# Kernel tuning notes

Hardware: AMD Instinct MI355X
Metric: run time of the kernel (lower is better)

Reference implementation:

```python
import jax, jax.numpy as jnp
import numpy as np

NUM_ENT = 14541; NUM_REL = 237; NUM_EDGES = 544230
D = 200; B = 2048
IPERM = 1; IK_H = 20; IK_W = 10; NFILT = 96; KER = 9
FLAT = IK_H * 2 * IK_W * NFILT * IPERM
LEAKY = 0.2; EPS = 1e-5


def _chequer_perm(rng):
    # faithful reimplementation of RagatInteractE.get_chequer_perm
    ent_perm = np.stack([rng.permutation(D) for _ in range(IPERM)])
    rel_perm = np.stack([rng.permutation(D) for _ in range(IPERM)])
    comb = []
    for k in range(IPERM):
        temp = []; ei = 0; ri = 0
        for i in range(IK_H):
            for j in range(IK_W):
                ent_first = (k % 2 == 0) == (i % 2 == 0)
                if ent_first:
                    temp.append(ent_perm[k, ei]); ei += 1
                    temp.append(rel_perm[k, ri] + D); ri += 1
                else:
                    temp.append(rel_perm[k, ri] + D); ri += 1
                    temp.append(ent_perm[k, ei]); ei += 1
        comb.append(temp)
    return jnp.asarray(np.asarray(comb, dtype=np.int32))


def _bn1d(x, g, b):  # [N, C], training-mode batch stats (torch default)
    m = x.mean(0); v = x.var(0)
    return (x - m) / jnp.sqrt(v + EPS) * g + b


def _bn2d(x, g, b):  # [N, C, H, W]
    m = x.mean((0, 2, 3), keepdims=True); v = x.var((0, 2, 3), keepdims=True)
    return (x - m) / jnp.sqrt(v + EPS) * g[None, :, None, None] + b[None, :, None, None]


def _seg_softmax_agg(score, msg, seg, n):
    # segment softmax over edges grouped by destination node, then weighted scatter-add
    mx = jax.ops.segment_max(score, seg, num_segments=n)
    ex = jnp.exp(score - mx[seg])
    den = jax.ops.segment_sum(ex, seg, num_segments=n)
    alpha = ex / (den[seg] + 1e-16)
    return jax.ops.segment_sum(msg * alpha[:, None], seg, num_segments=n)


def setup_inputs() -> dict:
    key = jax.random.key(0)
    ks = jax.random.split(key, 20)
    f = lambda k, shp, s=0.1: jax.random.normal(k, shp, jnp.float32) * s
    rng = np.random.RandomState(0)
    return {
        'init_embed': f(ks[0], (NUM_ENT, D)),
        'init_rel': f(ks[1], (2 * NUM_REL, D)),
        'loop_rel': f(ks[2], (1, D)),
        'w_in': f(ks[3], (D, D)),
        'w_out': f(ks[4], (D, D)),
        'w_loop': f(ks[5], (D, D)),
        'w_rel': f(ks[6], (D, D)),
        'att_in': f(ks[7], (D,)),
        'att_out': f(ks[8], (D,)),
        'bn_conv_g': jnp.ones((D,), jnp.float32),
        'bn_conv_b': jnp.zeros((D,), jnp.float32),
        'conv_filt': f(ks[9], (NFILT, 1, KER, KER)),
        'bn0_g': jnp.ones((IPERM,), jnp.float32),
        'bn0_b': jnp.zeros((IPERM,), jnp.float32),
        'bn1_g': jnp.ones((NFILT * IPERM,), jnp.float32),
        'bn1_b': jnp.zeros((NFILT * IPERM,), jnp.float32),
        'fc_w': f(ks[10], (FLAT, D), 0.02),
        'fc_b': jnp.zeros((D,), jnp.float32),
        'bn2_g': jnp.ones((D,), jnp.float32),
        'bn2_b': jnp.zeros((D,), jnp.float32),
        'bias': jnp.zeros((NUM_ENT,), jnp.float32),
        'edge_index': jax.random.randint(ks[11], (2, NUM_EDGES), 0, NUM_ENT, jnp.int32),
        'edge_type': jnp.concatenate([
            jax.random.randint(ks[12], (NUM_EDGES // 2,), 0, NUM_REL, jnp.int32),
            jax.random.randint(ks[13], (NUM_EDGES // 2,), NUM_REL, 2 * NUM_REL, jnp.int32)]),
        'sub': jax.random.randint(ks[14], (B,), 0, NUM_ENT, jnp.int32),
        'rel': jax.random.randint(ks[15], (B,), 0, 2 * NUM_REL, jnp.int32),
        'chequer_perm': _chequer_perm(rng),
    }


def reference(init_embed, init_rel, loop_rel, w_in, w_out, w_loop, w_rel,
              att_in, att_out, bn_conv_g, bn_conv_b, conv_filt,
              bn0_g, bn0_b, bn1_g, bn1_b, fc_w, fc_b, bn2_g, bn2_b, bias,
              edge_index, edge_type, sub, rel, chequer_perm):
    # --- RagatConv (1 layer): relation-aware composition + edge attention + scatter-agg ---
    rel_full = jnp.concatenate([init_rel, loop_rel], 0)
    src, dst = edge_index[0], edge_index[1]
    comp = init_embed[dst] * rel_full[edge_type]          # [E, D] mult composition
    half = NUM_EDGES // 2
    msg_in = comp[:half] @ w_in                           # [E/2, D]
    msg_out = comp[half:] @ w_out
    s_in = jax.nn.leaky_relu((msg_in * att_in).sum(-1), LEAKY)
    s_out = jax.nn.leaky_relu((msg_out * att_out).sum(-1), LEAKY)
    agg_in = _seg_softmax_agg(s_in, msg_in, src[:half], NUM_ENT)
    agg_out = _seg_softmax_agg(s_out, msg_out, src[half:], NUM_ENT)
    loop_msg = (init_embed * loop_rel[0]) @ w_loop
    ent = (agg_in + agg_out + loop_msg) / 3.0
    ent = jnp.tanh(_bn1d(ent, bn_conv_g, bn_conv_b))      # [num_ent, D]
    rel_out = init_rel @ w_rel                            # [2*num_rel, D]

    # --- InteractE chequer-perm circular-conv scoring ---
    comb = jnp.concatenate([ent[sub], rel_out[rel]], 1)   # [B, 2D]
    cheq = comb[:, chequer_perm]                          # [B, IPERM, 2D]
    x = cheq.reshape(B, IPERM, 2 * IK_W, IK_H)
    x = _bn2d(x, bn0_g, bn0_b)
    p = KER // 2
    x = jnp.concatenate([x[..., -p:, :], x, x[..., :p, :]], axis=2)  # circular pad H
    x = jnp.concatenate([x[..., -p:], x, x[..., :p]], axis=3)        # circular pad W
    kern = jnp.tile(conv_filt, (IPERM, 1, 1, 1))          # [NFILT*IPERM, 1, K, K]
    x = jax.lax.conv_general_dilated(x, kern, (1, 1), 'VALID',
                                     dimension_numbers=('NCHW', 'OIHW', 'NCHW'),
                                     feature_group_count=IPERM)       # [B, 96, 20, 20]
    x = jax.nn.relu(_bn2d(x, bn1_g, bn1_b))
    x = x.reshape(B, FLAT)
    x = x @ fc_w + fc_b
    x = jax.nn.relu(_bn1d(x, bn2_g, bn2_b))               # [B, D]
    scores = x @ ent.T + bias                              # one_to_n scoring
    return jax.nn.sigmoid(scores)
```

## Files before the change

kernel.cpp:

```cpp
#include <hip/hip_runtime.h>
#include <hip/hip_bf16.h>

constexpr int DV     = 200;
constexpr int N_ENT  = 14541;
constexpr int N_EDGE = 544230;
constexpr int HALF_E = N_EDGE / 2;
constexpr int NSEG   = 2 * N_ENT;
constexpr int BB     = 2048;
constexpr int NF     = 96;
constexpr int FLATN  = 38400;
constexpr float LEAK = 0.2f;
constexpr float BEPS = 1e-5f;

typedef unsigned int u32;
typedef unsigned short u16;
typedef __attribute__((ext_vector_type(8))) short bf16x8;
typedef __attribute__((ext_vector_type(4))) float f32x4;
typedef __attribute__((ext_vector_type(4))) unsigned short u16x4;

constexpr size_t OFF_S    = 0;
constexpr size_t OFF_EID  = 544230;
constexpr size_t OFF_CNT  = 1088460;
constexpr size_t OFF_OFFS = 1117542;
constexpr size_t OFF_AGG  = 1146624;
constexpr size_t OFF_FC   = 6963218;
constexpr size_t ZERO_BEG = OFF_CNT;
constexpr size_t ZERO_END = OFF_FC + 409600;
constexpr size_t OFF_V    = 7372818;
constexpr size_t OFF_WTH  = 0;
constexpr size_t OFF_ENTH = 3840000;
constexpr size_t OFF_ENTL = 5352264;
constexpr size_t OFF_WTL  = 7373220;
constexpr size_t OFF_EMB  = 7373218;
constexpr size_t OFF_EPRE = 10281418;
constexpr size_t OFF_ENT  = 13189618;
constexpr size_t OFF_RELO = 16097818;
constexpr size_t OFF_CM   = 16192618;
constexpr size_t OFF_CV   = 16192818;
constexpr size_t OFF_CHEQ = 16193018;
constexpr size_t OFF_YH   = 16193020;
constexpr size_t OFF_YL   = 16406012;
constexpr size_t OFF_P0   = 17012218;
constexpr size_t OFF_ST0  = 17016314;
constexpr size_t OFF_CHP  = 17016316;
constexpr size_t OFF_B1SC = 17409532;
constexpr size_t OFF_B1BI = 17409628;
constexpr size_t OFF_XC   = 17819324;
constexpr size_t WS_WORDS = OFF_XC + 39321600;

__device__ inline float bf2f(u16 u) { return __uint_as_float(((u32)u) << 16); }
__device__ inline u16 f2bf(float f) {
    __hip_bfloat16 h = __float2bfloat16(f);
    return *reinterpret_cast<u16*>(&h);
}
__device__ inline void gl_lds16(const void* g, void* l) {
    __builtin_amdgcn_global_load_lds(
        (const __attribute__((address_space(1))) void*)g,
        (__attribute__((address_space(3))) void*)l, 16, 0, 0);
}

__global__ void k_vatt(const float* __restrict__ w_in, const float* __restrict__ w_out,
                       const float* __restrict__ att_in, const float* __restrict__ att_out,
                       float* __restrict__ v) {
    int t = blockIdx.x * 256 + threadIdx.x;
    if (t < DV) {
        float s = 0.f;
        for (int j = 0; j < DV; ++j) s += w_in[t * DV + j] * att_in[j];
        v[t] = s;
    } else if (t < 2 * DV) {
        int k = t - DV;
        float s = 0.f;
        for (int j = 0; j < DV; ++j) s += w_out[k * DV + j] * att_out[j];
        v[t] = s;
    }
}

__global__ void k_edge_score(const float* __restrict__ embed, const float* __restrict__ rel,
                             const int* __restrict__ eidx, const int* __restrict__ etype,
                             const float* __restrict__ v, float* __restrict__ s_all) {
    int gw = (blockIdx.x * 256 + threadIdx.x) >> 6;
    int lane = threadIdx.x & 63;
    if (gw >= N_EDGE) return;
    int e = gw;
    int dst = eidx[N_EDGE + e], et = etype[e];
    int dir = (e >= HALF_E);
    const float* vv = v + dir * DV;
    const float* er = embed + (size_t)dst * DV;
    const float* rr = rel + (size_t)et * DV;
    float acc = 0.f;
    for (int d = lane; d < DV; d += 64) acc += er[d] * rr[d] * vv[d];
    for (int off = 32; off > 0; off >>= 1) acc += __shfl_down(acc, off);
    if (lane == 0) {
        float s = acc > 0.f ? acc : LEAK * acc;
        s_all[e] = s;
    }
}

__global__ void k_hist(const int* __restrict__ eidx, u32* __restrict__ cnt) {
    int e = blockIdx.x * 256 + threadIdx.x;
    if (e >= N_EDGE) return;
    int seg = (e >= HALF_E ? N_ENT : 0) + eidx[e];
    atomicAdd(&cnt[seg], 1u);
}

__global__ void k_scan(u32* __restrict__ cnt, u32* __restrict__ offs) {
    __shared__ u32 s[256];
    __shared__ u32 base;
    if (threadIdx.x == 0) base = 0;
    __syncthreads();
    for (int c0 = 0; c0 < NSEG; c0 += 256) {
        int i = c0 + threadIdx.x;
        u32 vv = (i < NSEG) ? cnt[i] : 0;
        s[threadIdx.x] = vv;
        __syncthreads();
        for (int o = 1; o < 256; o <<= 1) {
            u32 t = (threadIdx.x >= (u32)o) ? s[threadIdx.x - o] : 0u;
            __syncthreads();
            s[threadIdx.x] += t;
            __syncthreads();
        }
        u32 exc = base + s[threadIdx.x] - vv;
        if (i < NSEG) { offs[i] = exc; cnt[i] = exc; }
        __syncthreads();
        if (threadIdx.x == 255) base += s[255];
        __syncthreads();
    }
}

__global__ void k_scatter(const int* __restrict__ eidx, u32* __restrict__ pos,
                          u32* __restrict__ eid) {
    int e = blockIdx.x * 256 + threadIdx.x;
    if (e >= N_EDGE) return;
    int seg = (e >= HALF_E ? N_ENT : 0) + eidx[e];
    u32 slot = atomicAdd(&pos[seg], 1u);
    eid[slot] = (u32)e;
}

__global__ void k_seg_agg(const float* __restrict__ embed, const float* __restrict__ rel,
                          const int* __restrict__ eidx, const int* __restrict__ etype,
                          const float* __restrict__ s_all, const u32* __restrict__ offs,
                          const u32* __restrict__ eid, float* __restrict__ aggC) {
    int gw = (blockIdx.x * 256 + threadIdx.x) >> 6;
    int lane = threadIdx.x & 63;
    if (gw >= NSEG) return;
    u32 beg = offs[gw];
    u32 end = (gw == NSEG - 1) ? (u32)N_EDGE : offs[gw + 1];
    int deg = (int)(end - beg);
    if (deg == 0) return;
    float m = -1e30f;
    for (int i = lane; i < deg; i += 64) m = fmaxf(m, s_all[eid[beg + i]]);
    for (int o = 32; o > 0; o >>= 1) m = fmaxf(m, __shfl_xor(m, o));
    float dsum = 0.f;
    for (int i = lane; i < deg; i += 64) dsum += expf(s_all[eid[beg + i]] - m);
    for (int o = 32; o > 0; o >>= 1) dsum += __shfl_xor(dsum, o);
    float inv = 1.f / (dsum + 1e-16f);
    float a0 = 0.f, a1 = 0.f, a2 = 0.f, a3 = 0.f;
    bool t3 = (lane < 8);
    for (int j = 0; j < deg; ++j) {
        int e = (int)eid[beg + j];
        float alpha = expf(s_all[e] - m) * inv;
        int dst = eidx[N_EDGE + e], et = etype[e];
        const float* er = embed + (size_t)dst * DV;
        const float* rr = rel + (size_t)et * DV;
        float p0 = er[lane] * rr[lane];
        float p1 = er[lane + 64] * rr[lane + 64];
        float p2 = er[lane + 128] * rr[lane + 128];
        float p3 = t3 ? er[lane + 192] * rr[lane + 192] : 0.f;
        a0 = fmaf(p0, alpha, a0);
        a1 = fmaf(p1, alpha, a1);
        a2 = fmaf(p2, alpha, a2);
        a3 = fmaf(p3, alpha, a3);
    }
    float* ag = aggC + (size_t)gw * DV;
    ag[lane] = a0;
    ag[lane + 64] = a1;
    ag[lane + 128] = a2;
    if (t3) ag[lane + 192] = a3;
}

__global__ void k_embloop(const float* __restrict__ embed, const float* __restrict__ lr,
                          float* __restrict__ outp) {
    size_t i = (size_t)blockIdx.x * 256 + threadIdx.x;
    if (i < (size_t)N_ENT * DV) outp[i] = embed[i] * lr[i % DV];
}

__global__ void gemm_nn(const float* __restrict__ A, const float* __restrict__ B,
                        float* __restrict__ C, int M, int N, int K, int beta) {
    __shared__ float As[16][65];
    __shared__ float Bs[16][64];
    int bm = blockIdx.x * 64, bn = blockIdx.y * 64;
    int tx = threadIdx.x & 15, ty = threadIdx.x >> 4;
    float acc[4][4] = {};
    for (int k0 = 0; k0 < K; k0 += 16) {
        for (int i = threadIdx.x; i < 1024; i += 256) {
            int m = i >> 4, k = i & 15;
            int gm = bm + m, gk = k0 + k;
            As[k][m] = (gm < M && gk < K) ? A[(size_t)gm * K + gk] : 0.f;
        }
        for (int i = threadIdx.x; i < 1024; i += 256) {
            int k = i >> 6, n = i & 63;
            int gk = k0 + k, gn = bn + n;
            Bs[k][n] = (gk < K && gn < N) ? B[(size_t)gk * N + gn] : 0.f;
        }
        __syncthreads();
#pragma unroll
        for (int k = 0; k < 16; ++k) {
            float a[4], bv[4];
#pragma unroll
            for (int i = 0; i < 4; i++) a[i] = As[k][ty * 4 + i];
#pragma unroll
            for (int j = 0; j < 4; j++) bv[j] = Bs[k][tx * 4 + j];
#pragma unroll
            for (int i = 0; i < 4; i++)
#pragma unroll
                for (int j = 0; j < 4; j++) acc[i][j] += a[i] * bv[j];
        }
        __syncthreads();
    }
#pragma unroll
    for (int i = 0; i < 4; i++) {
        int r = bm + ty * 4 + i;
        if (r >= M) continue;
#pragma unroll
        for (int j = 0; j < 4; j++) {
            int c = bn + tx * 4 + j;
            if (c >= N) continue;
            size_t idx = (size_t)r * N + c;
            C[idx] = beta ? C[idx] + acc[i][j] : acc[i][j];
        }
    }
}

__global__ void k_colstats(const float* __restrict__ X, int R,
                           float* __restrict__ cm, float* __restrict__ cv) {
    int col = blockIdx.x;
    __shared__ float rs[256], rss[256];
    float s = 0.f, ss = 0.f;
    for (int r = threadIdx.x; r < R; r += 256) {
        float x = X[(size_t)r * DV + col];
        s += x; ss += x * x;
    }
    rs[threadIdx.x] = s; rss[threadIdx.x] = ss;
    __syncthreads();
    for (int o = 128; o > 0; o >>= 1) {
        if (threadIdx.x < o) { rs[threadIdx.x] += rs[threadIdx.x + o]; rss[threadIdx.x] += rss[threadIdx.x + o]; }
        __syncthreads();
    }
    if (threadIdx.x == 0) {
        float m = rs[0] / R;
        cm[col] = m;
        cv[col] = rss[0] / R - m * m;
    }
}

__global__ void k_bn_ent(const float* __restrict__ epre, const float* __restrict__ cm,
                         const float* __restrict__ cv, const float* __restrict__ g,
                         const float* __restrict__ b, float* __restrict__ ent,
                         u16* __restrict__ eh, u16* __restrict__ el) {
    size_t i = (size_t)blockIdx.x * 256 + threadIdx.x;
    if (i >= (size_t)N_ENT * 208) return;
    int row = (int)(i / 208), col = (int)(i % 208);
    if (col < DV) {
        float val = (epre[(size_t)row * DV + col] - cm[col]) * rsqrtf(cv[col] + 9.f * BEPS) * g[col] + b[col];
        val = tanhf(val);
        ent[(size_t)row * DV + col] = val;
        u16 h = f2bf(val);
        eh[i] = h;
        el[i] = f2bf(val - bf2f(h));
    } else { eh[i] = 0; el[i] = 0; }
}

__global__ void k_bn2y(const float* __restrict__ fc, const float* __restrict__ cm,
                       const float* __restrict__ cv, const float* __restrict__ g,
                       const float* __restrict__ b, u16* __restrict__ yh,
                       u16* __restrict__ yl) {
    size_t i = (size_t)blockIdx.x * 256 + threadIdx.x;
    if (i >= (size_t)BB * 208) return;
    int row = (int)(i / 208), col = (int)(i % 208);
    if (col < DV) {
        float val = (fc[(size_t)row * DV + col] - cm[col]) * rsqrtf(cv[col] + BEPS) * g[col] + b[col];
        val = fmaxf(val, 0.f);
        u16 h = f2bf(val);
        yh[i] = h;
        yl[i] = f2bf(val - bf2f(h));
    } else { yh[i] = 0; yl[i] = 0; }
}

__global__ __launch_bounds__(256) void k_wt(const float* __restrict__ W,
                                            u16* __restrict__ Wth, u16* __restrict__ Wtl) {
    __shared__ float lds[64][65];
    int k0 = blockIdx.x * 64, n0 = blockIdx.y * 64;
    for (int idx = threadIdx.x; idx < 4096; idx += 256) {
        int kl = idx >> 6, nl = idx & 63;
        int gk = k0 + kl, gn = n0 + nl;
        lds[kl][nl] = (gn < DV) ? W[(size_t)gk * DV + gn] : 0.f;
    }
    __syncthreads();
    int nl = threadIdx.x >> 2, kq = threadIdx.x & 3;
    int gn = n0 + nl;
    if (gn >= DV) return;
    size_t base = (size_t)gn * FLATN + k0 + kq * 16;
    bf16x8 vh0, vh1, vl0, vl1;
#pragma unroll
    for (int j = 0; j < 8; ++j) {
        float w0 = lds[kq * 16 + j][nl];
        u16 h0 = f2bf(w0);
        vh0[j] = (short)h0; vl0[j] = (short)f2bf(w0 - bf2f(h0));
        float w1 = lds[kq * 16 + 8 + j][nl];
        u16 h1 = f2bf(w1);
        vh1[j] = (short)h1; vl1[j] = (short)f2bf(w1 - bf2f(h1));
    }
    *reinterpret_cast<bf16x8*>(Wth + base)     = vh0;
    *reinterpret_cast<bf16x8*>(Wth + base + 8) = vh1;
    *reinterpret_cast<bf16x8*>(Wtl + base)     = vl0;
    *reinterpret_cast<bf16x8*>(Wtl + base + 8) = vl1;
}

__global__ void k_cheq(const float* __restrict__ ent, const float* __restrict__ rel_out,
                       const int* __restrict__ sub, const int* __restrict__ rel,
                       const int* __restrict__ perm, float* __restrict__ cheq,
                       float* __restrict__ p0) {
    int b = blockIdx.x;
    int sb = sub[b], rb = rel[b];
    __shared__ float rs[256], rss[256];
    float s = 0.f, ss = 0.f;
    for (int i = threadIdx.x; i < 400; i += 256) {
        int p = perm[i];
        float v = (p < DV) ? ent[(size_t)sb * DV + p] : rel_out[(size_t)rb * DV + (p - DV)];
        cheq[(size_t)b * 400 + i] = v;
        s += v; ss += v * v;
    }
    rs[threadIdx.x] = s; rss[threadIdx.x] = ss;
    __syncthreads();
    for (int o = 128; o > 0; o >>= 1) {
        if (threadIdx.x < o) { rs[threadIdx.x] += rs[threadIdx.x + o]; rss[threadIdx.x] += rss[threadIdx.x + o]; }
        __syncthreads();
    }
    if (threadIdx.x == 0) { p0[b] = rs[0]; p0[BB + b] = rss[0]; }
}

__global__ void k_red_bn0(const float* __restrict__ p0, float* __restrict__ st) {
    __shared__ float rs[256], rss[256];
    float s = 0.f, ss = 0.f;
    for (int i = threadIdx.x; i < BB; i += 256) { s += p0[i]; ss += p0[BB + i]; }
    rs[threadIdx.x] = s; rss[threadIdx.x] = ss;
    __syncthreads();
    for (int o = 128; o > 0; o >>= 1) {
        if (threadIdx.x < o) { rs[threadIdx.x] += rs[threadIdx.x + o]; rss[threadIdx.x] += rss[threadIdx.x + o]; }
        __syncthreads();
    }
    if (threadIdx.x == 0) { st[0] = rs[0]; st[1] = rss[0]; }
}

__global__ __launch_bounds__(384, 4) void k_conv(const float* __restrict__ cheq,
                                              const float* __restrict__ st,
                                              const float* __restrict__ g0, const float* __restrict__ b0,
                                              const float* __restrict__ filt,
                                              __hip_bfloat16* __restrict__ xconv,
                                              float* __restrict__ chp) {
    int t = threadIdx.x;
    int img = t / 192;
    int tl = t - img * 192;
    int b = blockIdx.x * 2 + img;
    __shared__ float pad[2][784];
    __shared__ float flds[7968];
    __shared__ float red[384];
    for (int i = t; i < 7776; i += 384) {
        int f = i / 81, q = i - f * 81;
        flds[f * 83 + q] = filt[i];
    }
    const float N0 = (float)BB * 400.f;
    float m = st[0] / N0;
    float va = st[1] / N0 - m * m;
    float sg = rsqrtf(va + BEPS) * g0[0];
    float sb = b0[0] - m * sg;
    for (int i = t; i < 1568; i += 384) {
        int im = i / 784, j = i - im * 784;
        int h = j / 28, w2 = j % 28;
        int r = (h + 16) % 20, c = (w2 + 16) % 20;
        pad[im][j] = cheq[(size_t)(blockIdx.x * 2 + im) * 400 + r * 20 + c] * sg + sb;
    }
    __syncthreads();
    int f = tl % 96, hp = tl / 96;
    const float* fbase = flds + f * 83;
    const float* mypad = pad[img];
    float cs = 0.f, css = 0.f;
    u16* xo = (u16*)xconv + (size_t)b * FLATN + f * 400 + hp * 200;
    for (int rt = 0; rt < 10; ++rt) {
        int y = hp * 10 + rt;
        float acc[20];
#pragma unroll
        for (int x = 0; x < 20; ++x) acc[x] = 0.f;
        for (int dy = 0; dy < 9; ++dy) {
            float pr[28];
            const float4* prow = reinterpret_cast<const float4*>(&mypad[(y + dy) * 28]);
#pragma unroll
            for (int qv = 0; qv < 7; ++qv) {
                float4 v4 = prow[qv];
                pr[qv * 4 + 0] = v4.x; pr[qv * 4 + 1] = v4.y;
                pr[qv * 4 + 2] = v4.z; pr[qv * 4 + 3] = v4.w;
            }
            float fw[9];
#pragma unroll
            for (int dx = 0; dx < 9; ++dx) fw[dx] = fbase[dy * 9 + dx];
#pragma unroll
            for (int dx = 0; dx < 9; ++dx)
#pragma unroll
                for (int x = 0; x < 20; ++x)
                    acc[x] = fmaf(pr[x + dx], fw[dx], acc[x]);
        }
#pragma unroll
        for (int x = 0; x < 20; ++x) { cs += acc[x]; css += acc[x] * acc[x]; }
#pragma unroll
        for (int jj = 0; jj < 5; ++jj) {
            u16x4 o;
#pragma unroll
            for (int q2 = 0; q2 < 4; ++q2) o[q2] = f2bf(acc[jj * 4 + q2]);
            *reinterpret_cast<u16x4*>(xo + rt * 20 + jj * 4) = o;
        }
    }
    red[t] = cs; __syncthreads();
    if (tl < 96) chp[(size_t)b * 192 + tl] = red[img * 192 + tl] + red[img * 192 + tl + 96];
    __syncthreads();
    red[t] = css; __syncthreads();
    if (tl < 96) chp[(size_t)b * 192 + 96 + tl] = red[img * 192 + tl] + red[img * 192 + tl + 96];
}

__global__ void k_bn1_final(const float* __restrict__ chp, const float* __restrict__ g1,
                            const float* __restrict__ b1, float* __restrict__ sc,
                            float* __restrict__ bi) {
    int c = blockIdx.x;
    __shared__ float rs[256], rss[256];
    float s = 0.f, ss = 0.f;
    for (int b = threadIdx.x; b < BB; b += 256) {
        s += chp[(size_t)b * 192 + c];
        ss += chp[(size_t)b * 192 + 96 + c];
    }
    rs[threadIdx.x] = s; rss[threadIdx.x] = ss;
    __syncthreads();
    for (int o = 128; o > 0; o >>= 1) {
        if (threadIdx.x < o) { rs[threadIdx.x] += rs[threadIdx.x + o]; rss[threadIdx.x] += rss[threadIdx.x + o]; }
        __syncthreads();
    }
    if (threadIdx.x == 0) {
        float N = (float)BB * 400.f;
        float m = rs[0] / N;
        float v = rss[0] / N - m * m;
        float s_ = rsqrtf(v + BEPS) * g1[c];
        sc[c] = s_;
        bi[c] = b1[c] - m * s_;
    }
}

__global__ __launch_bounds__(256) void k_fc_mfma(const u16* __restrict__ X,
        const u16* __restrict__ Wth, const u16* __restrict__ Wtl,
        const float* __restrict__ sc, const float* __restrict__ bi,
        float* __restrict__ outp) {
    __shared__ __align__(16) char blds[53248];
    int tid = threadIdx.x;
    int w = tid >> 6, lane = tid & 63;
    int lrow = lane & 15, lkg = lane >> 4;
    int mw = blockIdx.x * 128 + w * 32;
    int kbase = blockIdx.y * 1280;
    f32x4 acc[2][13] = {};
    for (int it = 0; it < 20; ++it) {
        int k0 = kbase + it * 64;
        __syncthreads();
        bf16x8 araw[2][2];
#pragma unroll
        for (int mf = 0; mf < 2; ++mf)
#pragma unroll
            for (int kt = 0; kt < 2; ++kt) {
                int r = mw + mf * 16 + lrow;
                int kk = k0 + kt * 32 + lkg * 8;
                araw[mf][kt] = *reinterpret_cast<const bf16x8*>(X + (size_t)r * FLATN + kk);
            }
#pragma unroll
        for (int q = 0; q < 7; ++q) {
            int bidx = q * 256 + w * 64;
            if (bidx < 1600) {
                int idx = bidx + lane;
                int n = idx >> 3;
                int slot = (idx & 7) ^ (n & 7);
                size_t gsrc = (size_t)n * FLATN + k0 + slot * 8;
                gl_lds16(Wth + gsrc, blds + bidx * 16);
                gl_lds16(Wtl + gsrc, blds + 26624 + bidx * 16);
            }
        }
        bf16x8 ah[2][2], al[2][2];
#pragma unroll
        for (int mf = 0; mf < 2; ++mf)
#pragma unroll
            for (int kt = 0; kt < 2; ++kt) {
                int kk = k0 + kt * 32 + lkg * 8;
                int c = kk / 400;
                float s_ = sc[c], b_ = bi[c];
                bf16x8 fh, fl;
#pragma unroll
                for (int j = 0; j < 8; ++j) {
                    float v = bf2f((u16)araw[mf][kt][j]);
                    v = fmaxf(fmaf(v, s_, b_), 0.f);
                    u16 h = f2bf(v);
                    fh[j] = (short)h;
                    fl[j] = (short)f2bf(v - bf2f(h));
                }
                ah[mf][kt] = fh;
                al[mf][kt] = fl;
            }
        __syncthreads();
#pragma unroll
        for (int nt = 0; nt < 13; ++nt) {
            int n = nt * 16 + lrow;
            int row = n * 128, nx = n & 7;
            int off0 = row + ((lkg ^ nx) << 4);
            int off1 = row + (((4 + lkg) ^ nx) << 4);
            bf16x8 bh0 = *reinterpret_cast<const bf16x8*>(blds + off0);
            bf16x8 bh1 = *reinterpret_cast<const bf16x8*>(blds + off1);
            bf16x8 bl0 = *reinterpret_cast<const bf16x8*>(blds + 26624 + off0);
            bf16x8 bl1 = *reinterpret_cast<const bf16x8*>(blds + 26624 + off1);
#pragma unroll
            for (int mf = 0; mf < 2; ++mf) {
                acc[mf][nt] = __builtin_amdgcn_mfma_f32_16x16x32_bf16(ah[mf][0], bh0, acc[mf][nt], 0, 0, 0);
                acc[mf][nt] = __builtin_amdgcn_mfma_f32_16x16x32_bf16(ah[mf][1], bh1, acc[mf][nt], 0, 0, 0);
                acc[mf][nt] = __builtin_amdgcn_mfma_f32_16x16x32_bf16(ah[mf][0], bl0, acc[mf][nt], 0, 0, 0);
                acc[mf][nt] = __builtin_amdgcn_mfma_f32_16x16x32_bf16(ah[mf][1], bl1, acc[mf][nt], 0, 0, 0);
                acc[mf][nt] = __builtin_amdgcn_mfma_f32_16x16x32_bf16(al[mf][0], bh0, acc[mf][nt], 0, 0, 0);
                acc[mf][nt] = __builtin_amdgcn_mfma_f32_16x16x32_bf16(al[mf][1], bh1, acc[mf][nt], 0, 0, 0);
            }
        }
    }
#pragma unroll
    for (int mf = 0; mf < 2; ++mf)
#pragma unroll
        for (int nt = 0; nt < 13; ++nt) {
            int col = nt * 16 + lrow;
            if (col < DV) {
#pragma unroll
                for (int i = 0; i < 4; ++i) {
                    int r = mw + mf * 16 + lkg * 4 + i;
                    unsafeAtomicAdd(&outp[(size_t)r * DV + col], acc[mf][nt][i]);
                }
            }
        }
}

__global__ __launch_bounds__(256) void k_sc_mfma(const u16* __restrict__ Yh, const u16* __restrict__ Yl,
        const u16* __restrict__ Eh, const u16* __restrict__ El,
        const float* __restrict__ bias, float* __restrict__ outp) {
    __shared__ __align__(16) char elds[32768];
    int tid = threadIdx.x;
    int w = tid >> 6, lane = tid & 63;
    int lrow = lane & 15, lkg = lane >> 4;
    int mw = blockIdx.x * 128 + w * 32;
    int bn = blockIdx.y * 256;
    f32x4 acc[2][16] = {};
    bf16x8 zv = {};
    for (int kt = 0; kt < 7; ++kt) {
        int kbase = kt * 32;
        __syncthreads();
        int kk = kbase + lkg * 8;
        bool kval = (kt < 6) || (lkg < 2);
        bf16x8 ah[2], al[2];
#pragma unroll
        for (int mf = 0; mf < 2; ++mf) {
            int r = mw + mf * 16 + lrow;
            size_t off = (size_t)r * 208 + kk;
            ah[mf] = kval ? *reinterpret_cast<const bf16x8*>(Yh + off) : zv;
            al[mf] = kval ? *reinterpret_cast<const bf16x8*>(Yl + off) : zv;
        }
#pragma unroll
        for (int q = 0; q < 4; ++q) {
            int bidx = q * 256 + w * 64;
            int idx = bidx + lane;
            int n = idx >> 2;
            int slot = (idx & 3) ^ (n & 3);
            int gn = bn + n; if (gn > N_ENT - 1) gn = N_ENT - 1;
            size_t gsrc = (size_t)gn * 208 + kbase + slot * 8;
            gl_lds16(Eh + gsrc, elds + bidx * 16);
            gl_lds16(El + gsrc, elds + 16384 + bidx * 16);
        }
        __syncthreads();
#pragma unroll
        for (int nt = 0; nt < 16; ++nt) {
            int n = nt * 16 + lrow;
            int off = n * 64 + ((lkg ^ (n & 3)) << 4);
            bf16x8 bh = *reinterpret_cast<const bf16x8*>(elds + off);
            bf16x8 bl = *reinterpret_cast<const bf16x8*>(elds + 16384 + off);
            acc[0][nt] = __builtin_amdgcn_mfma_f32_16x16x32_bf16(ah[0], bh, acc[0][nt], 0, 0, 0);
            acc[0][nt] = __builtin_amdgcn_mfma_f32_16x16x32_bf16(ah[0], bl, acc[0][nt], 0, 0, 0);
            acc[0][nt] = __builtin_amdgcn_mfma_f32_16x16x32_bf16(al[0], bh, acc[0][nt], 0, 0, 0);
            acc[1][nt] = __builtin_amdgcn_mfma_f32_16x16x32_bf16(ah[1], bh, acc[1][nt], 0, 0, 0);
            acc[1][nt] = __builtin_amdgcn_mfma_f32_16x16x32_bf16(ah[1], bl, acc[1][nt], 0, 0, 0);
            acc[1][nt] = __builtin_amdgcn_mfma_f32_16x16x32_bf16(al[1], bh, acc[1][nt], 0, 0, 0);
        }
    }
#pragma unroll
    for (int mf = 0; mf < 2; ++mf)
#pragma unroll
        for (int nt = 0; nt < 16; ++nt) {
            int col = bn + nt * 16 + lrow;
            if (col < N_ENT) {
                float bv = bias[col];
#pragma unroll
                for (int i = 0; i < 4; ++i) {
                    int r = mw + mf * 16 + lkg * 4 + i;
                    float s = acc[mf][nt][i] + bv;
                    outp[(size_t)r * N_ENT + col] = 1.f / (1.f + expf(-s));
                }
            }
        }
}

extern "C" void kernel_launch(void* const* d_in, const int* in_sizes, int n_in,
                              void* d_out, int out_size, void* d_ws, size_t ws_size,
                              hipStream_t stream) {
    const float* init_embed = (const float*)d_in[0];
    const float* init_rel   = (const float*)d_in[1];
    const float* loop_rel   = (const float*)d_in[2];
    const float* w_in   = (const float*)d_in[3];
    const float* w_out  = (const float*)d_in[4];
    const float* w_loop = (const float*)d_in[5];
    const float* w_rel  = (const float*)d_in[6];
    const float* att_in  = (const float*)d_in[7];
    const float* att_out = (const float*)d_in[8];
    const float* bnc_g = (const float*)d_in[9];
    const float* bnc_b = (const float*)d_in[10];
    const float* filt  = (const float*)d_in[11];
    const float* g0 = (const float*)d_in[12];
    const float* b0 = (const float*)d_in[13];
    const float* g1 = (const float*)d_in[14];
    const float* b1 = (const float*)d_in[15];
    const float* fc_w = (const float*)d_in[16];
    const float* g2 = (const float*)d_in[18];
    const float* b2 = (const float*)d_in[19];
    const float* bias = (const float*)d_in[20];
    const int* eidx  = (const int*)d_in[21];
    const int* etype = (const int*)d_in[22];
    const int* sub   = (const int*)d_in[23];
    const int* rel   = (const int*)d_in[24];
    const int* perm  = (const int*)d_in[25];

    float* ws = (float*)d_ws;
    float* outp = (float*)d_out;
    if (ws_size < WS_WORDS * sizeof(float)) return;

    float* s_all  = ws + OFF_S;
    u32*   eid    = (u32*)(ws + OFF_EID);
    u32*   cnt    = (u32*)(ws + OFF_CNT);
    u32*   offs   = (u32*)(ws + OFF_OFFS);
    float* aggC   = ws + OFF_AGG;
    float* fc_out = ws + OFF_FC;
    float* v      = ws + OFF_V;
    float* embl   = ws + OFF_EMB;
    float* epre   = ws + OFF_EPRE;
    float* ent    = ws + OFF_ENT;
    float* relo   = ws + OFF_RELO;
    float* cm     = ws + OFF_CM;
    float* cv     = ws + OFF_CV;
    float* cheq   = ws + OFF_CHEQ;
    float* p0     = ws + OFF_P0;
    float* st0    = ws + OFF_ST0;
    float* chp    = ws + OFF_CHP;
    float* b1sc   = ws + OFF_B1SC;
    float* b1bi   = ws + OFF_B1BI;
    u16*   Wth    = (u16*)(ws + OFF_WTH);
    u16*   Wtl    = (u16*)(ws + OFF_WTL);
    u16*   entH   = (u16*)(ws + OFF_ENTH);
    u16*   entL   = (u16*)(ws + OFF_ENTL);
    u16*   Yh     = (u16*)(ws + OFF_YH);
    u16*   Yl     = (u16*)(ws + OFF_YL);
    __hip_bfloat16* xconv = (__hip_bfloat16*)(ws + OFF_XC);

    hipMemsetAsync(ws + ZERO_BEG, 0, (ZERO_END - ZERO_BEG) * sizeof(float), stream);

    k_vatt<<<2, 256, 0, stream>>>(w_in, w_out, att_in, att_out, v);

    int edge_wave_blocks = (N_EDGE + 3) / 4;
    k_edge_score<<<edge_wave_blocks, 256, 0, stream>>>(init_embed, init_rel, eidx, etype, v, s_all);

    int eb = (N_EDGE + 255) / 256;
    k_hist<<<eb, 256, 0, stream>>>(eidx, cnt);
    k_scan<<<1, 256, 0, stream>>>(cnt, offs);
    k_scatter<<<eb, 256, 0, stream>>>(eidx, cnt, eid);
    k_seg_agg<<<(NSEG + 3) / 4, 256, 0, stream>>>(init_embed, init_rel, eidx, etype,
                                                  s_all, offs, eid, aggC);

    k_embloop<<<((size_t)N_ENT * DV + 255) / 256, 256, 0, stream>>>(init_embed, loop_rel, embl);

    dim3 gE((N_ENT + 63) / 64, (DV + 63) / 64);
    gemm_nn<<<gE, 256, 0, stream>>>(aggC,                       w_in,   epre, N_ENT, DV, DV, 0);
    gemm_nn<<<gE, 256, 0, stream>>>(aggC + (size_t)N_ENT * DV,  w_out,  epre, N_ENT, DV, DV, 1);
    gemm_nn<<<gE, 256, 0, stream>>>(embl,                       w_loop, epre, N_ENT, DV, DV, 1);
    dim3 gR((474 + 63) / 64, (DV + 63) / 64);
    gemm_nn<<<gR, 256, 0, stream>>>(init_rel, w_rel, relo, 474, DV, DV, 0);

    k_colstats<<<DV, 256, 0, stream>>>(epre, N_ENT, cm, cv);
    k_bn_ent<<<((size_t)N_ENT * 208 + 255) / 256, 256, 0, stream>>>(
        epre, cm, cv, bnc_g, bnc_b, ent, entH, entL);

    dim3 gW(FLATN / 64, 4);
    k_wt<<<gW, 256, 0, stream>>>(fc_w, Wth, Wtl);

    k_cheq<<<BB, 256, 0, stream>>>(ent, relo, sub, rel, perm, cheq, p0);
    k_red_bn0<<<1, 256, 0, stream>>>(p0, st0);
    k_conv<<<BB / 2, 384, 0, stream>>>(cheq, st0, g0, b0, filt, xconv, chp);
    k_bn1_final<<<NF, 256, 0, stream>>>(chp, g1, b1, b1sc, b1bi);

    dim3 gFC(16, 30);
    k_fc_mfma<<<gFC, 256, 0, stream>>>((const u16*)xconv, Wth, Wtl, b1sc, b1bi, fc_out);

    k_colstats<<<DV, 256, 0, stream>>>(fc_out, BB, cm, cv);
    k_bn2y<<<((size_t)BB * 208 + 255) / 256, 256, 0, stream>>>(fc_out, cm, cv, g2, b2, Yh, Yl);

    dim3 gS(16, 57);
    k_sc_mfma<<<gS, 256, 0, stream>>>(Yh, Yl, entH, entL, bias, outp);
}
```

Baseline: 1.224 ms.

## Fuse three entity projection GEMMs into one split-bf16 MFMA kernel

Replaces the three scalar fp32 tiled GEMMs (in, out, loop) and the separate embed*loop_rel elementwise kernel with a single MFMA kernel. It accumulates all three products in registers, using hi/lo bf16 splitting (three MFMAs per tile) to approximate fp32 precision. A small pre-kernel transposes and splits the three weight matrices into bf16 hi/lo with K padded to 224. This removes the intermediate embl buffer, the read-modify-write of epre across launches, and two launches, at the cost of slightly reduced precision and a workspace region overlapping the cheq buffer.

```diff
diff --git a/kernel.cpp b/kernel.cpp
--- a/kernel.cpp
+++ b/kernel.cpp
@@ -31,13 +31,14 @@
 constexpr size_t OFF_ENTH = 3840000;
 constexpr size_t OFF_ENTL = 5352264;
 constexpr size_t OFF_WTL  = 7373220;
-constexpr size_t OFF_EMB  = 7373218;
 constexpr size_t OFF_EPRE = 10281418;
 constexpr size_t OFF_ENT  = 13189618;
 constexpr size_t OFF_RELO = 16097818;
 constexpr size_t OFF_CM   = 16192618;
 constexpr size_t OFF_CV   = 16192818;
 constexpr size_t OFF_CHEQ = 16193018;
+constexpr size_t OFF_WT3H = 16193018;
+constexpr size_t OFF_WT3L = 16261118;
 constexpr size_t OFF_YH   = 16193020;
 constexpr size_t OFF_YL   = 16406012;
 constexpr size_t OFF_P0   = 17012218;
@@ -178,12 +179,6 @@
     if (t3) ag[lane + 192] = a3;
 }
 
-__global__ void k_embloop(const float* __restrict__ embed, const float* __restrict__ lr,
-                          float* __restrict__ outp) {
-    size_t i = (size_t)blockIdx.x * 256 + threadIdx.x;
-    if (i < (size_t)N_ENT * DV) outp[i] = embed[i] * lr[i % DV];
-}
-
 __global__ void gemm_nn(const float* __restrict__ A, const float* __restrict__ B,
                         float* __restrict__ C, int M, int N, int K, int beta) {
     __shared__ float As[16][65];
@@ -229,6 +224,100 @@
             C[idx] = beta ? C[idx] + acc[i][j] : acc[i][j];
         }
     }
+}
+
+__global__ void k_wt3(const float* __restrict__ w_in, const float* __restrict__ w_out,
+                      const float* __restrict__ w_loop,
+                      u16* __restrict__ wTh, u16* __restrict__ wTl) {
+    int i = blockIdx.x * 256 + threadIdx.x;
+    if (i >= 3 * 200 * 224) return;
+    int s = i / 44800, rem = i - s * 44800;
+    int n = rem / 224, k = rem - n * 224;
+    const float* w = (s == 0) ? w_in : (s == 1 ? w_out : w_loop);
+    float v = (k < 200) ? w[k * 200 + n] : 0.f;
+    u16 h = f2bf(v);
+    wTh[i] = h;
+    wTl[i] = f2bf(v - bf2f(h));
+}
+
+__global__ __launch_bounds__(256) void k_epre_mfma(const float* __restrict__ aggC,
+        const float* __restrict__ embed, const float* __restrict__ lr,
+        const u16* __restrict__ wTh, const u16* __restrict__ wTl,
+        float* __restrict__ epre) {
+    __shared__ __align__(16) char elds[26624];
+    int tid = threadIdx.x;
+    int w = tid >> 6, lane = tid & 63;
+    int lrow = lane & 15, lkg = lane >> 4;
+    int mw = blockIdx.x * 128 + w * 32;
+    f32x4 acc[2][13] = {};
+    for (int seg = 0; seg < 3; ++seg) {
+        const float* Asrc = (seg == 0) ? aggC : (seg == 1 ? aggC + (size_t)N_ENT * DV : embed);
+        const u16* bhg = wTh + seg * 44800;
+        const u16* blg = wTl + seg * 44800;
+        for (int kt = 0; kt < 7; ++kt) {
+            int kb = kt * 32;
+            __syncthreads();
+            int kk = kb + lkg * 8;
+            bool kval = (kt < 6) || (lkg < 1);
+            bf16x8 ah[2], al[2];
+#pragma unroll
+            for (int mf = 0; mf < 2; ++mf) {
+                int r = mw + mf * 16 + lrow; if (r > N_ENT - 1) r = N_ENT - 1;
+                bf16x8 vh = {}, vl = {};
+                if (kval) {
+                    const float* ap = Asrc + (size_t)r * DV + kk;
+#pragma unroll
+                    for (int j = 0; j < 8; ++j) {
+                        float v = ap[j];
+                        if (seg == 2) v *= lr[kk + j];
+                        u16 h = f2bf(v);
+                        vh[j] = (short)h;
+                        vl[j] = (short)f2bf(v - bf2f(h));
+                    }
+                }
+                ah[mf] = vh; al[mf] = vl;
+            }
+#pragma unroll
+            for (int q = 0; q < 4; ++q) {
+                int bidx = q * 256 + w * 64;
+                if (bidx < 832) {
+                    int idx = bidx + lane;
+                    int n = idx >> 2;
+                    int slot = (idx & 3) ^ (n & 3);
+                    size_t gsrc = (size_t)n * 224 + kb + slot * 8;
+                    gl_lds16(bhg + gsrc, elds + bidx * 16);
+                    gl_lds16(blg + gsrc, elds + 13312 + bidx * 16);
+                }
+            }
+            __syncthreads();
+#pragma unroll
+            for (int nt = 0; nt < 13; ++nt) {
+                int n = nt * 16 + lrow;
+                int off = n * 64 + ((lkg ^ (n & 3)) << 4);
+                bf16x8 bh = *reinterpret_cast<const bf16x8*>(elds + off);
+                bf16x8 bl = *reinterpret_cast<const bf16x8*>(elds + 13312 + off);
+#pragma unroll
+                for (int mf = 0; mf < 2; ++mf) {
+                    acc[mf][nt] = __builtin_amdgcn_mfma_f32_16x16x32_bf16(ah[mf], bh, acc[mf][nt], 0, 0, 0);
+                    acc[mf][nt] = __builtin_amdgcn_mfma_f32_16x16x32_bf16(ah[mf], bl, acc[mf][nt], 0, 0, 0);
+                    acc[mf][nt] = __builtin_amdgcn_mfma_f32_16x16x32_bf16(al[mf], bh, acc[mf][nt], 0, 0, 0);
+                }
+            }
+        }
+    }
+#pragma unroll
+    for (int mf = 0; mf < 2; ++mf)
+#pragma unroll
+        for (int nt = 0; nt < 13; ++nt) {
+            int col = nt * 16 + lrow;
+            if (col < DV) {
+#pragma unroll
+                for (int i = 0; i < 4; ++i) {
+                    int r = mw + mf * 16 + lkg * 4 + i;
+                    if (r < N_ENT) epre[(size_t)r * DV + col] = acc[mf][nt][i];
+                }
+            }
+        }
 }
 
 __global__ void k_colstats(const float* __restrict__ X, int R,
@@ -495,17 +584,17 @@
                 int kk = k0 + kt * 32 + lkg * 8;
                 int c = kk / 400;
                 float s_ = sc[c], b_ = bi[c];
-                bf16x8 fh, fl;
+                bf16x8 fh2, fl2;
 #pragma unroll
                 for (int j = 0; j < 8; ++j) {
                     float v = bf2f((u16)araw[mf][kt][j]);
                     v = fmaxf(fmaf(v, s_, b_), 0.f);
                     u16 h = f2bf(v);
-                    fh[j] = (short)h;
-                    fl[j] = (short)f2bf(v - bf2f(h));
+                    fh2[j] = (short)h;
+                    fl2[j] = (short)f2bf(v - bf2f(h));
                 }
-                ah[mf][kt] = fh;
-                al[mf][kt] = fl;
+                ah[mf][kt] = fh2;
+                al[mf][kt] = fl2;
             }
         __syncthreads();
 #pragma unroll
@@ -651,7 +740,6 @@
     float* aggC   = ws + OFF_AGG;
     float* fc_out = ws + OFF_FC;
     float* v      = ws + OFF_V;
-    float* embl   = ws + OFF_EMB;
     float* epre   = ws + OFF_EPRE;
     float* ent    = ws + OFF_ENT;
     float* relo   = ws + OFF_RELO;
@@ -665,6 +753,8 @@
     float* b1bi   = ws + OFF_B1BI;
     u16*   Wth    = (u16*)(ws + OFF_WTH);
     u16*   Wtl    = (u16*)(ws + OFF_WTL);
+    u16*   wT3h   = (u16*)(ws + OFF_WT3H);
+    u16*   wT3l   = (u16*)(ws + OFF_WT3L);
     u16*   entH   = (u16*)(ws + OFF_ENTH);
     u16*   entL   = (u16*)(ws + OFF_ENTL);
     u16*   Yh     = (u16*)(ws + OFF_YH);
@@ -674,6 +764,7 @@
     hipMemsetAsync(ws + ZERO_BEG, 0, (ZERO_END - ZERO_BEG) * sizeof(float), stream);
 
     k_vatt<<<2, 256, 0, stream>>>(w_in, w_out, att_in, att_out, v);
+    k_wt3<<<(3 * 200 * 224 + 255) / 256, 256, 0, stream>>>(w_in, w_out, w_loop, wT3h, wT3l);
 
     int edge_wave_blocks = (N_EDGE + 3) / 4;
     k_edge_score<<<edge_wave_blocks, 256, 0, stream>>>(init_embed, init_rel, eidx, etype, v, s_all);
@@ -685,12 +776,9 @@
     k_seg_agg<<<(NSEG + 3) / 4, 256, 0, stream>>>(init_embed, init_rel, eidx, etype,
                                                   s_all, offs, eid, aggC);
 
-    k_embloop<<<((size_t)N_ENT * DV + 255) / 256, 256, 0, stream>>>(init_embed, loop_rel, embl);
-
-    dim3 gE((N_ENT + 63) / 64, (DV + 63) / 64);
-    gemm_nn<<<gE, 256, 0, stream>>>(aggC,                       w_in,   epre, N_ENT, DV, DV, 0);
-    gemm_nn<<<gE, 256, 0, stream>>>(aggC + (size_t)N_ENT * DV,  w_out,  epre, N_ENT, DV, DV, 1);
-    gemm_nn<<<gE, 256, 0, stream>>>(embl,                       w_loop, epre, N_ENT, DV, DV, 1);
+    k_epre_mfma<<<(N_ENT + 127) / 128, 256, 0, stream>>>(aggC, init_embed, loop_rel,
+                                                         wT3h, wT3l, epre);
+
     dim3 gR((474 + 63) / 64, (DV + 63) / 64);
     gemm_nn<<<gR, 256, 0, stream>>>(init_rel, w_rel, relo, 474, DV, DV, 0);
 
```

Result: faster. 1.152 ms (-5.9%).
